# Performance work log

Hardware: AMD Instinct MI355X
Metric: run time of the kernel (lower is better)

## Reference

```python
import jax, jax.numpy as jnp
import numpy as np

LMBDA = 0.25  # from init_kwargs


def setup_inputs() -> dict:
    key = jax.random.key(0)
    k1, k2 = jax.random.split(key)
    N, K, D = 131072, 512, 256
    embeddings = jax.random.normal(k1, (N, D), dtype=jnp.float32)
    centroids = jax.random.normal(k2, (K, D), dtype=jnp.float32)
    return {"embeddings": embeddings, "centroids": centroids}


def reference(embeddings, centroids):
    # distances[n,k] = lmbda * sum_d (e[n,d] - c[k,d])^2
    # expanded form avoids materializing the [N,K,D] broadcast intermediate:
    # |e-c|^2 = |e|^2 + |c|^2 - 2 e.c
    e_sq = jnp.sum(embeddings * embeddings, axis=1)  # [N]
    c_sq = jnp.sum(centroids * centroids, axis=1)    # [K]
    cross = jnp.einsum('nd,kd->nk', embeddings, centroids)  # [N,K]
    distances = LMBDA * (e_sq[:, None] + c_sq[None, :] - 2.0 * cross)  # [N,K]
    cluster_distances = jnp.max(distances, axis=1)          # [N]
    cluster_assignments = jnp.argmax(distances, axis=1)     # [N], int
    loss = LMBDA * jnp.sum(cluster_distances)  # note: lmbda applied twice, as in source
    return loss, jax.lax.stop_gradient(cluster_assignments)
```

## Files before the change

kernel.cpp:

```cpp
#include <hip/hip_runtime.h>

#define ND 256
#define NK 512
#define LM2 0.0625f
#define DELTA 0.25f

typedef _Float16 f16x8 __attribute__((ext_vector_type(8)));
typedef float f32x4 __attribute__((ext_vector_type(4)));
typedef unsigned short u16x8 __attribute__((ext_vector_type(8)));
typedef unsigned short u16x4 __attribute__((ext_vector_type(4)));

#define GLD16(GSRC, LDST)                                                      \
    __builtin_amdgcn_global_load_lds(                                         \
        (const __attribute__((address_space(1))) void*)(GSRC),                \
        (__attribute__((address_space(3))) void*)(LDST), 16, 0, 0)

__global__ __launch_bounds__(64) void prep_kernel(const float* __restrict__ Cg,
                                                  float* __restrict__ csq,
                                                  unsigned short* __restrict__ Cf) {
    const int k = blockIdx.x, lane = threadIdx.x;
    float4 v = *(const float4*)(Cg + (size_t)k * ND + lane * 4);
    float s = v.x * v.x + v.y * v.y + v.z * v.z + v.w * v.w;
#pragma unroll
    for (int m = 1; m <= 32; m <<= 1) s += __shfl_xor(s, m, 64);
    if (lane == 0) csq[k] = s;
    u16x4 h;
    h[0] = __builtin_bit_cast(unsigned short, (_Float16)v.x);
    h[1] = __builtin_bit_cast(unsigned short, (_Float16)v.y);
    h[2] = __builtin_bit_cast(unsigned short, (_Float16)v.z);
    h[3] = __builtin_bit_cast(unsigned short, (_Float16)v.w);
    const int panel = k >> 6, col = k & 63;
    const int krow = (lane >> 3) * 4 + ((lane >> 1) & 3);
    const size_t idx = ((size_t)panel << 14) + ((((size_t)krow << 6) + col) << 3) + ((lane & 1) << 2);
    *(u16x4*)(Cf + idx) = h;
}

__global__ __launch_bounds__(512, 2) void kmeans_mfma(
    const float* __restrict__ E, const unsigned short* __restrict__ Cf,
    const float* __restrict__ csq, uint2* __restrict__ partials,
    float* __restrict__ e2s) {
    __shared__ unsigned short Bbuf[2][16384];

    const int tid = threadIdx.x;
    const int lane = tid & 63, wid = tid >> 6;
    const int l15 = lane & 15, l4 = lane >> 4;
    const int rowbase = blockIdx.x << 8;
    const int wrow = rowbase + wid * 32;

#pragma unroll
    for (int i = 0; i < 4; ++i)
        GLD16(Cf + (((size_t)(wid * 4 + i) * 64 + lane) << 3),
              &Bbuf[0][(size_t)(wid * 4 + i) << 9]);

    const float* a0 = E + (size_t)(wrow + l15) * ND + l4 * 8;
    const float* a1 = E + (size_t)(wrow + 16 + l15) * ND + l4 * 8;

    f16x8 A[2][8];
    float e2 = 0.f;
#pragma unroll
    for (int m = 0; m < 2; ++m) {
        const float* ap = m ? a1 : a0;
#pragma unroll
        for (int half = 0; half < 2; ++half) {
            float4 t[8];
#pragma unroll
            for (int q = 0; q < 4; ++q) {
                t[q * 2]     = *(const float4*)(ap + (half * 4 + q) * 32);
                t[q * 2 + 1] = *(const float4*)(ap + (half * 4 + q) * 32 + 4);
            }
#pragma unroll
            for (int q = 0; q < 4; ++q) {
                float4 v0 = t[q * 2], v1 = t[q * 2 + 1];
                e2 += v0.x * v0.x + v0.y * v0.y + v0.z * v0.z + v0.w * v0.w +
                      v1.x * v1.x + v1.y * v1.y + v1.z * v1.z + v1.w * v1.w;
                u16x8 h;
                h[0] = __builtin_bit_cast(unsigned short, (_Float16)v0.x);
                h[1] = __builtin_bit_cast(unsigned short, (_Float16)v0.y);
                h[2] = __builtin_bit_cast(unsigned short, (_Float16)v0.z);
                h[3] = __builtin_bit_cast(unsigned short, (_Float16)v0.w);
                h[4] = __builtin_bit_cast(unsigned short, (_Float16)v1.x);
                h[5] = __builtin_bit_cast(unsigned short, (_Float16)v1.y);
                h[6] = __builtin_bit_cast(unsigned short, (_Float16)v1.z);
                h[7] = __builtin_bit_cast(unsigned short, (_Float16)v1.w);
                A[m][half * 4 + q] = __builtin_bit_cast(f16x8, h);
            }
        }
    }

    unsigned k1[2][4], k2[2][4];
#pragma unroll
    for (int m = 0; m < 2; ++m)
#pragma unroll
        for (int j = 0; j < 4; ++j) { k1[m][j] = 0u; k2[m][j] = 0u; }

    const unsigned ckb = (unsigned)(NK - 1) - (unsigned)l15;

#pragma unroll 1
    for (int p = 0; p < 8; ++p) {
        __syncthreads();
        if (p < 7) {
            const unsigned short* gsrc = Cf + ((size_t)(p + 1) << 14);
            unsigned short* ldst = (unsigned short*)Bbuf[(p + 1) & 1];
#pragma unroll
            for (int i = 0; i < 4; ++i)
                GLD16(gsrc + (((size_t)(wid * 4 + i) * 64 + lane) << 3),
                      &ldst[(size_t)(wid * 4 + i) << 9]);
        }
        float csp[4];
#pragma unroll
        for (int n = 0; n < 4; ++n) csp[n] = csq[(p << 6) + n * 16 + l15];

        const unsigned short* cur = Bbuf[p & 1];
        f32x4 acc[2][4] = {};
#pragma unroll
        for (int ks = 0; ks < 8; ++ks) {
#pragma unroll
            for (int n = 0; n < 4; ++n) {
                const u16x8 bfr =
                    *(const u16x8*)&cur[(size_t)((((ks << 2) + l4) << 6) + n * 16 + l15) << 3];
                const f16x8 bf = __builtin_bit_cast(f16x8, bfr);
                acc[0][n] = __builtin_amdgcn_mfma_f32_16x16x32_f16(A[0][ks], bf, acc[0][n], 0, 0, 0);
                acc[1][n] = __builtin_amdgcn_mfma_f32_16x16x32_f16(A[1][ks], bf, acc[1][n], 0, 0, 0);
            }
        }
#pragma unroll
        for (int m = 0; m < 2; ++m)
#pragma unroll
            for (int j = 0; j < 4; ++j)
#pragma unroll
                for (int n = 0; n < 4; ++n) {
                    const float s = fmaf(-2.f, acc[m][n][j], csp[n]);
                    const unsigned b = __builtin_bit_cast(unsigned, s);
                    const unsigned mono = b ^ ((unsigned)((int)b >> 31) | 0x80000000u);
                    const unsigned key = (mono & 0xFFFFFE00u) | (ckb - (unsigned)((p << 6) + n * 16));
                    const unsigned mn = min(k1[m][j], key);
                    k1[m][j] = max(k1[m][j], key);
                    k2[m][j] = max(k2[m][j], mn);
                }
    }

#pragma unroll
    for (int m = 0; m < 2; ++m)
#pragma unroll
        for (int j = 0; j < 4; ++j) {
            unsigned a = k1[m][j], b2 = k2[m][j];
#pragma unroll
            for (int mk = 1; mk <= 8; mk <<= 1) {
                const unsigned oa = __shfl_xor(a, mk, 64);
                const unsigned ob = __shfl_xor(b2, mk, 64);
                const unsigned mn = min(a, oa);
                a = max(a, oa);
                b2 = max(max(b2, ob), mn);
            }
            if (l15 == 0) {
                const int row = wrow + m * 16 + l4 * 4 + j;
                uint2 o;
                o.x = a;
                o.y = b2;
                partials[row] = o;
            }
        }

#pragma unroll
    for (int mk = 1; mk <= 32; mk <<= 1) e2 += __shfl_xor(e2, mk, 64);
    if (lane == 0) e2s[blockIdx.x * 8 + wid] = e2;
}

__global__ __launch_bounds__(256) void combine_kernel(
    const uint2* __restrict__ partials, const float* __restrict__ csq,
    const float* __restrict__ E, const float* __restrict__ Cg,
    float* __restrict__ out, float* __restrict__ sum2) {
    const int n = blockIdx.x * 256 + threadIdx.x;
    const uint2 kk = partials[n];
    const unsigned m1 = kk.x & 0xFFFFFE00u;
    float v1 = __builtin_bit_cast(float, (m1 & 0x80000000u) ? (m1 ^ 0x80000000u) : ~m1);
    int i1 = (int)(NK - 1) - (int)(kk.x & 511u);
    const unsigned m2 = kk.y & 0xFFFFFE00u;
    const float v2 = __builtin_bit_cast(float, (m2 & 0x80000000u) ? (m2 ^ 0x80000000u) : ~m2);
    const int i2 = (int)(NK - 1) - (int)(kk.y & 511u);

    if (v1 - v2 <= DELTA) {
        const float* e = E + (size_t)n * ND;
        const float* c1p = Cg + (size_t)i1 * ND;
        const float* c2p = Cg + (size_t)i2 * ND;
        float d1 = 0.f, d2 = 0.f;
        for (int d = 0; d < ND; d += 4) {
            float4 ev = *(const float4*)(e + d);
            float4 cv1 = *(const float4*)(c1p + d);
            float4 cv2 = *(const float4*)(c2p + d);
            d1 += ev.x * cv1.x + ev.y * cv1.y + ev.z * cv1.z + ev.w * cv1.w;
            d2 += ev.x * cv2.x + ev.y * cv2.y + ev.z * cv2.z + ev.w * cv2.w;
        }
        const float s1 = csq[i1] - 2.f * d1;
        const float s2 = csq[i2] - 2.f * d2;
        if (s2 > s1 || (s2 == s1 && i2 < i1)) { v1 = s2; i1 = i2; } else { v1 = s1; }
    }
    out[1 + n] = (float)i1;
    float s = v1;
#pragma unroll
    for (int mk = 1; mk <= 32; mk <<= 1) s += __shfl_xor(s, mk, 64);
    __shared__ float wsm[4];
    const int lane = threadIdx.x & 63, wd = threadIdx.x >> 6;
    if (lane == 0) wsm[wd] = s;
    __syncthreads();
    if (threadIdx.x == 0) sum2[blockIdx.x] = wsm[0] + wsm[1] + wsm[2] + wsm[3];
}

__global__ __launch_bounds__(256) void final_kernel(const float* __restrict__ e2s,
                                                    const float* __restrict__ sum2,
                                                    float* __restrict__ out) {
    float s = 0.f;
    for (int i = threadIdx.x; i < 4096; i += 256) s += e2s[i];
    for (int i = threadIdx.x; i < 512; i += 256) s += sum2[i];
#pragma unroll
    for (int mk = 1; mk <= 32; mk <<= 1) s += __shfl_xor(s, mk, 64);
    __shared__ float wsm[4];
    const int lane = threadIdx.x & 63, wd = threadIdx.x >> 6;
    if (lane == 0) wsm[wd] = s;
    __syncthreads();
    if (threadIdx.x == 0) out[0] = LM2 * (wsm[0] + wsm[1] + wsm[2] + wsm[3]);
}

extern "C" void kernel_launch(void* const* d_in, const int* in_sizes, int n_in,
                              void* d_out, int out_size, void* d_ws, size_t ws_size,
                              hipStream_t stream) {
    (void)n_in; (void)out_size; (void)ws_size;
    const float* E = (const float*)d_in[0];
    const float* Cg = (const float*)d_in[1];
    float* out = (float*)d_out;

    float* wsf = (float*)d_ws;
    float* csq = wsf;
    float* e2s = wsf + 512;
    float* sum2 = wsf + 4608;
    unsigned short* Cf = (unsigned short*)(wsf + 5120);
    uint2* partials = (uint2*)(wsf + 5120 + 65536);

    const int N = in_sizes[0] / ND;
    const int nblk = N >> 8;

    prep_kernel<<<NK, 64, 0, stream>>>(Cg, csq, Cf);
    kmeans_mfma<<<nblk, 512, 0, stream>>>(E, Cf, csq, partials, e2s);
    combine_kernel<<<N / 256, 256, 0, stream>>>(partials, csq, E, Cg, out, sum2);
    final_kernel<<<1, 256, 0, stream>>>(e2s, sum2, out);
}
```

Measured before the change: 105.1 us.

## Swap MFMA operands so centroids index rows, shrinking per-row top-2 state

Transposes the MFMA so centroid fragments are the A operand and embedding rows the B operand. Each lane's accumulator then holds four centroids of one embedding row, so the per-row top-2 keys shrink from 16 registers to 4 per lane. The cross-lane reduction drops from four shuffle stages to two. Loop order also changes to finish one 16-centroid column group at a time, which lowers accumulator pressure from 8 to 2 f32x4 and lets csq be read as one float4.

```diff
diff --git a/kernel.cpp b/kernel.cpp
--- a/kernel.cpp
+++ b/kernel.cpp
@@ -52,14 +52,11 @@
         GLD16(Cf + (((size_t)(wid * 4 + i) * 64 + lane) << 3),
               &Bbuf[0][(size_t)(wid * 4 + i) << 9]);
 
-    const float* a0 = E + (size_t)(wrow + l15) * ND + l4 * 8;
-    const float* a1 = E + (size_t)(wrow + 16 + l15) * ND + l4 * 8;
-
-    f16x8 A[2][8];
+    f16x8 Ef[2][8];
     float e2 = 0.f;
 #pragma unroll
-    for (int m = 0; m < 2; ++m) {
-        const float* ap = m ? a1 : a0;
+    for (int g = 0; g < 2; ++g) {
+        const float* ap = E + (size_t)(wrow + g * 16 + l15) * ND + l4 * 8;
 #pragma unroll
         for (int half = 0; half < 2; ++half) {
             float4 t[8];
@@ -82,18 +79,12 @@
                 h[5] = __builtin_bit_cast(unsigned short, (_Float16)v1.y);
                 h[6] = __builtin_bit_cast(unsigned short, (_Float16)v1.z);
                 h[7] = __builtin_bit_cast(unsigned short, (_Float16)v1.w);
-                A[m][half * 4 + q] = __builtin_bit_cast(f16x8, h);
-            }
-        }
-    }
-
-    unsigned k1[2][4], k2[2][4];
-#pragma unroll
-    for (int m = 0; m < 2; ++m)
-#pragma unroll
-        for (int j = 0; j < 4; ++j) { k1[m][j] = 0u; k2[m][j] = 0u; }
-
-    const unsigned ckb = (unsigned)(NK - 1) - (unsigned)l15;
+                Ef[g][half * 4 + q] = __builtin_bit_cast(f16x8, h);
+            }
+        }
+    }
+
+    unsigned k1[2] = {0u, 0u}, k2[2] = {0u, 0u};
 
 #pragma unroll 1
     for (int p = 0; p < 8; ++p) {
@@ -106,60 +97,56 @@
                 GLD16(gsrc + (((size_t)(wid * 4 + i) * 64 + lane) << 3),
                       &ldst[(size_t)(wid * 4 + i) << 9]);
         }
-        float csp[4];
-#pragma unroll
-        for (int n = 0; n < 4; ++n) csp[n] = csq[(p << 6) + n * 16 + l15];
-
         const unsigned short* cur = Bbuf[p & 1];
-        f32x4 acc[2][4] = {};
-#pragma unroll
-        for (int ks = 0; ks < 8; ++ks) {
-#pragma unroll
-            for (int n = 0; n < 4; ++n) {
+#pragma unroll
+        for (int n = 0; n < 4; ++n) {
+            const float4 csp = *(const float4*)(csq + (p << 6) + n * 16 + l4 * 4);
+            f32x4 a0 = {}, a1 = {};
+#pragma unroll
+            for (int ks = 0; ks < 8; ++ks) {
                 const u16x8 bfr =
                     *(const u16x8*)&cur[(size_t)((((ks << 2) + l4) << 6) + n * 16 + l15) << 3];
-                const f16x8 bf = __builtin_bit_cast(f16x8, bfr);
-                acc[0][n] = __builtin_amdgcn_mfma_f32_16x16x32_f16(A[0][ks], bf, acc[0][n], 0, 0, 0);
-                acc[1][n] = __builtin_amdgcn_mfma_f32_16x16x32_f16(A[1][ks], bf, acc[1][n], 0, 0, 0);
-            }
-        }
-#pragma unroll
-        for (int m = 0; m < 2; ++m)
-#pragma unroll
-            for (int j = 0; j < 4; ++j)
-#pragma unroll
-                for (int n = 0; n < 4; ++n) {
-                    const float s = fmaf(-2.f, acc[m][n][j], csp[n]);
+                const f16x8 cf = __builtin_bit_cast(f16x8, bfr);
+                a0 = __builtin_amdgcn_mfma_f32_16x16x32_f16(cf, Ef[0][ks], a0, 0, 0, 0);
+                a1 = __builtin_amdgcn_mfma_f32_16x16x32_f16(cf, Ef[1][ks], a1, 0, 0, 0);
+            }
+            const unsigned kbase = (unsigned)(NK - 1 - ((p << 6) + n * 16 + l4 * 4));
+            const float cs[4] = {csp.x, csp.y, csp.z, csp.w};
+#pragma unroll
+            for (int g = 0; g < 2; ++g) {
+                const f32x4 ag = g ? a1 : a0;
+#pragma unroll
+                for (int j = 0; j < 4; ++j) {
+                    const float s = fmaf(-2.f, ag[j], cs[j]);
                     const unsigned b = __builtin_bit_cast(unsigned, s);
                     const unsigned mono = b ^ ((unsigned)((int)b >> 31) | 0x80000000u);
-                    const unsigned key = (mono & 0xFFFFFE00u) | (ckb - (unsigned)((p << 6) + n * 16));
-                    const unsigned mn = min(k1[m][j], key);
-                    k1[m][j] = max(k1[m][j], key);
-                    k2[m][j] = max(k2[m][j], mn);
+                    const unsigned key = (mono & 0xFFFFFE00u) | (kbase - (unsigned)j);
+                    const unsigned mn = min(k1[g], key);
+                    k1[g] = max(k1[g], key);
+                    k2[g] = max(k2[g], mn);
                 }
-    }
-
-#pragma unroll
-    for (int m = 0; m < 2; ++m)
-#pragma unroll
-        for (int j = 0; j < 4; ++j) {
-            unsigned a = k1[m][j], b2 = k2[m][j];
-#pragma unroll
-            for (int mk = 1; mk <= 8; mk <<= 1) {
-                const unsigned oa = __shfl_xor(a, mk, 64);
-                const unsigned ob = __shfl_xor(b2, mk, 64);
-                const unsigned mn = min(a, oa);
-                a = max(a, oa);
-                b2 = max(max(b2, ob), mn);
-            }
-            if (l15 == 0) {
-                const int row = wrow + m * 16 + l4 * 4 + j;
-                uint2 o;
-                o.x = a;
-                o.y = b2;
-                partials[row] = o;
-            }
-        }
+            }
+        }
+    }
+
+#pragma unroll
+    for (int g = 0; g < 2; ++g) {
+        unsigned a = k1[g], b2 = k2[g];
+#pragma unroll
+        for (int mk = 16; mk <= 32; mk <<= 1) {
+            const unsigned oa = __shfl_xor(a, mk, 64);
+            const unsigned ob = __shfl_xor(b2, mk, 64);
+            const unsigned mn = min(a, oa);
+            a = max(a, oa);
+            b2 = max(max(b2, ob), mn);
+        }
+        if (l4 == 0) {
+            uint2 o;
+            o.x = a;
+            o.y = b2;
+            partials[wrow + g * 16 + l15] = o;
+        }
+    }
 
 #pragma unroll
     for (int mk = 1; mk <= 32; mk <<= 1) e2 += __shfl_xor(e2, mk, 64);
```

Result: faster. 90.20 us (median of 2 runs) (-14.2%).
